# Optimization experiments

Hardware: AMD Instinct MI355X
Metric: run time of the kernel (lower is better)

Reference implementation:

```python
import jax, jax.numpy as jnp
import numpy as np


def setup_inputs() -> dict:
    key = jax.random.key(0)
    ks = jax.random.split(key, 7)
    B, D, d1, d2, d3 = 256, 256, 1024, 512, 256
    s = lambda f: 1.0 / np.sqrt(f)  # torch nn.Linear-style init scale
    return {
        "x": jax.random.normal(ks[0], (B, D), jnp.float32),
        "W1": jax.random.normal(ks[1], (d1, D), jnp.float32) * s(D),
        "b1": jax.random.normal(ks[2], (d1,), jnp.float32) * s(D),
        "W2": jax.random.normal(ks[3], (d2, d1), jnp.float32) * s(d1),
        "b2": jax.random.normal(ks[4], (d2,), jnp.float32) * s(d1),
        "W3": jax.random.normal(ks[5], (d3, d2), jnp.float32) * s(d2),
        "b3": jax.random.normal(ks[6], (d3,), jnp.float32) * s(d2),
        "k": 10,
    }


def _border_dists(x, W1, b1, W2, b2, W3, b3):
    # Layer 1: pre-activations and boundary distances. For the first layer the
    # effective linear map is W1 itself (shared across the batch).
    z1 = x @ W1.T + b1                                   # [B, d1]
    dist1 = jnp.abs(z1) / jnp.linalg.norm(W1, axis=1)    # [B, d1]
    m1 = (z1 > 0).astype(x.dtype)
    V1 = m1[:, :, None] * W1[None]                       # [B, d1, D] per-instance map after ReLU
    h1 = m1 * z1

    # Layer 2
    z2 = h1 @ W2.T + b2                                  # [B, d2]
    V2 = jnp.einsum('oi,bid->bod', W2, V1)               # [B, d2, D]
    dist2 = jnp.abs(z2) / jnp.linalg.norm(V2, axis=2)
    m2 = (z2 > 0).astype(x.dtype)
    h2 = m2 * z2

    # Layer 3
    z3 = h2 @ W3.T + b3                                  # [B, d3]
    V3 = jnp.einsum('oi,bid->bod', W3, m2[:, :, None] * V2)  # [B, d3, D]
    dist3 = jnp.abs(z3) / jnp.linalg.norm(V3, axis=2)

    return jnp.concatenate([dist1, dist2, dist3], axis=1)  # [B, d1+d2+d3]


def reference(x, W1, b1, W2, b2, W3, b3, k):
    dists = _border_dists(x, W1, b1, W2, b2, W3, b3)
    # smallest-k distances per instance via top_k on negated distances
    neg_top, _ = jax.lax.top_k(-dists, k)                # [B, k]
    return jnp.sum(-neg_top)                             # border-distance loss (scalar)
```

## Files before the change

kernel.cpp:

```cpp
#include <hip/hip_runtime.h>
#include <math.h>
#include <float.h>

#define B   256
#define D   256
#define D1  1024
#define D2  512
#define D3  256
#define NDIST (D1 + D2 + D3)
#define CQ  2.0f

typedef __attribute__((ext_vector_type(8))) short short8;
typedef __attribute__((ext_vector_type(4))) float f32x4;
typedef __attribute__((ext_vector_type(4))) int   i32x4;

__device__ __forceinline__ float waveReduceSum(float v) {
    #pragma unroll
    for (int off = 32; off > 0; off >>= 1)
        v += __shfl_down(v, off, 64);
    return v;
}
__device__ __forceinline__ float waveReduceMax(float v) {
    #pragma unroll
    for (int off = 32; off > 0; off >>= 1)
        v = fmaxf(v, __shfl_down(v, off, 64));
    return v;
}
__device__ __forceinline__ unsigned short f2bf(float f) {
    unsigned int u = __float_as_uint(f);
    u = (u + 0x7FFFu + ((u >> 16) & 1u)) >> 16;
    return (unsigned short)u;
}
__device__ __forceinline__ float bf2f(unsigned short h) {
    return __uint_as_float(((unsigned int)h) << 16);
}
__device__ __forceinline__ void gld16(const void* g, void* l) {
    __builtin_amdgcn_global_load_lds(
        (const __attribute__((address_space(1))) unsigned int*)g,
        (__attribute__((address_space(3))) unsigned int*)l, 16, 0, 0);
}
__device__ __forceinline__ int swz_src(int row, int lane) {
    return ((lane & 3) + ((row >> 1) & 3)) & 3;
}
__device__ __forceinline__ int swz_frag(int row, int quad) {
    return row * 32 + (((quad - ((row >> 1) & 3)) & 3) * 8);
}

__device__ __forceinline__ void split8(const float* p, short8& h8, short8& l8) {
    float4 a = *(const float4*)(p);
    float4 b = *(const float4*)(p + 4);
    float hv[8] = { a.x, a.y, a.z, a.w, b.x, b.y, b.z, b.w };
    #pragma unroll
    for (int q = 0; q < 8; q++) {
        unsigned short hh = f2bf(hv[q]);
        h8[q] = (short)hh;
        l8[q] = (short)f2bf(hv[q] - bf2f(hh));
    }
}

template <int KD, int KL>
__device__ __forceinline__ void mfma3_64(
    const unsigned short* __restrict__ Ahi, const unsigned short* __restrict__ Alo,
    const unsigned short* __restrict__ Bhi, const unsigned short* __restrict__ Blo,
    int m0, int n0, int k0, unsigned short* sm, f32x4 acc[2][2]) {
    int tid = threadIdx.x;
    int l = tid & 63, w = tid >> 6;
    int rsub = l >> 2;
    int quad = l >> 4, l16 = l & 15;
    int wm = (w >> 1) * 32, wn = (w & 1) * 32;
    unsigned short* sAh = sm;
    unsigned short* sAl = sm + 2048;
    unsigned short* sBh = sm + 4096;
    unsigned short* sBl = sm + 6144;
    ptrdiff_t dA = Alo - Ahi, dB = Blo - Bhi;
    int rloc = w * 16 + rsub;
    int c = swz_src(rloc, l);
    const unsigned short* pa = Ahi + (size_t)(m0 + rloc) * KD + k0 + c * 8;
    const unsigned short* pb = Bhi + (size_t)(n0 + rloc) * KD + k0 + c * 8;
    int aoff[2], boff[2];
    #pragma unroll
    for (int mt = 0; mt < 2; mt++) aoff[mt] = swz_frag(wm + mt * 16 + l16, quad);
    #pragma unroll
    for (int nt = 0; nt < 2; nt++) boff[nt] = swz_frag(wn + nt * 16 + l16, quad);
    for (int kk = 0; kk < KL; kk += 32) {
        gld16(pa + kk,      sAh + w * 512);
        gld16(pa + dA + kk, sAl + w * 512);
        gld16(pb + kk,      sBh + w * 512);
        gld16(pb + dB + kk, sBl + w * 512);
        __syncthreads();
        short8 ah[2], al[2], bh[2], bl[2];
        #pragma unroll
        for (int mt = 0; mt < 2; mt++) {
            ah[mt] = *(const short8*)(sAh + aoff[mt]);
            al[mt] = *(const short8*)(sAl + aoff[mt]);
        }
        #pragma unroll
        for (int nt = 0; nt < 2; nt++) {
            bh[nt] = *(const short8*)(sBh + boff[nt]);
            bl[nt] = *(const short8*)(sBl + boff[nt]);
        }
        #pragma unroll
        for (int mt = 0; mt < 2; mt++)
            #pragma unroll
            for (int nt = 0; nt < 2; nt++) {
                acc[mt][nt] = __builtin_amdgcn_mfma_f32_16x16x32_bf16(ah[mt], bh[nt], acc[mt][nt], 0, 0, 0);
                acc[mt][nt] = __builtin_amdgcn_mfma_f32_16x16x32_bf16(ah[mt], bl[nt], acc[mt][nt], 0, 0, 0);
                acc[mt][nt] = __builtin_amdgcn_mfma_f32_16x16x32_bf16(al[mt], bh[nt], acc[mt][nt], 0, 0, 0);
            }
        __syncthreads();
    }
}

__global__ __launch_bounds__(256) void k_l1p(
    const float* __restrict__ x, const float* __restrict__ W1,
    const float* __restrict__ W2, const float* __restrict__ W3,
    const float* __restrict__ b1,
    float* __restrict__ dists, unsigned char* __restrict__ m1q,
    unsigned short* __restrict__ h1hi, unsigned short* __restrict__ h1lo,
    float* __restrict__ zeros, float* __restrict__ outp,
    unsigned short* __restrict__ W2hi, unsigned short* __restrict__ W2lo,
    unsigned short* __restrict__ W3hi, unsigned short* __restrict__ W3lo,
    signed char* __restrict__ W1Ti8, float* __restrict__ saq,
    signed char* __restrict__ W2i8,  float* __restrict__ sbq,
    signed char* __restrict__ W3i8,  float* __restrict__ s3q,
    float* __restrict__ rn1) {
    __shared__ __align__(16) unsigned short sm[8192];
    int blk = blockIdx.x;
    int t = threadIdx.x;

    if (blk < 64) {
        unsigned short* sAh = sm;
        unsigned short* sAl = sm + 2048;
        unsigned short* sBh = sm + 4096;
        unsigned short* sBl = sm + 6144;
        int m0 = (blk & 3) * 64, n0 = (blk >> 2) * 64;
        int l = t & 63, w = t >> 6;
        int rsub = l >> 2;
        int quad = l >> 4, l16 = l & 15;
        int wm = (w >> 1) * 32, wn = (w & 1) * 32;
        int rloc = w * 16 + rsub;
        int c = swz_src(rloc, l);
        const float* pax = x + (size_t)(m0 + rloc) * D + c * 8;
        const float* pbw = W1 + (size_t)(n0 + rloc) * D + c * 8;
        int aoff[2], boff[2];
        #pragma unroll
        for (int mt = 0; mt < 2; mt++) aoff[mt] = swz_frag(wm + mt * 16 + l16, quad);
        #pragma unroll
        for (int nt = 0; nt < 2; nt++) boff[nt] = swz_frag(wn + nt * 16 + l16, quad);
        int wrA = w * 512 + l * 8;
        f32x4 acc[2][2] = {};
        for (int kk = 0; kk < D; kk += 32) {
            short8 ha, la, hb, lb;
            split8(pax + kk, ha, la);
            split8(pbw + kk, hb, lb);
            *(short8*)(sAh + wrA) = ha;
            *(short8*)(sAl + wrA) = la;
            *(short8*)(sBh + wrA) = hb;
            *(short8*)(sBl + wrA) = lb;
            __syncthreads();
            short8 ah[2], al[2], bh[2], bl[2];
            #pragma unroll
            for (int mt = 0; mt < 2; mt++) {
                ah[mt] = *(const short8*)(sAh + aoff[mt]);
                al[mt] = *(const short8*)(sAl + aoff[mt]);
            }
            #pragma unroll
            for (int nt = 0; nt < 2; nt++) {
                bh[nt] = *(const short8*)(sBh + boff[nt]);
                bl[nt] = *(const short8*)(sBl + boff[nt]);
            }
            #pragma unroll
            for (int mt = 0; mt < 2; mt++)
                #pragma unroll
                for (int nt = 0; nt < 2; nt++) {
                    acc[mt][nt] = __builtin_amdgcn_mfma_f32_16x16x32_bf16(ah[mt], bh[nt], acc[mt][nt], 0, 0, 0);
                    acc[mt][nt] = __builtin_amdgcn_mfma_f32_16x16x32_bf16(ah[mt], bl[nt], acc[mt][nt], 0, 0, 0);
                    acc[mt][nt] = __builtin_amdgcn_mfma_f32_16x16x32_bf16(al[mt], bh[nt], acc[mt][nt], 0, 0, 0);
                }
            __syncthreads();
        }
        #pragma unroll
        for (int mt = 0; mt < 2; mt++)
            #pragma unroll
            for (int nt = 0; nt < 2; nt++) {
                int n = n0 + wn + nt * 16 + l16;
                float bv = b1[n];
                #pragma unroll
                for (int r = 0; r < 4; r++) {
                    int m = m0 + wm + mt * 16 + quad * 4 + r;
                    float z = acc[mt][nt][r] + bv;
                    size_t idx = (size_t)m * D1 + n;
                    dists[idx] = fabsf(z);
                    m1q[idx] = (z > 0.f) ? 0xFFu : 0u;
                    float h = z > 0.f ? z : 0.f;
                    unsigned short hh = f2bf(h);
                    h1hi[idx] = hh;
                    h1lo[idx] = f2bf(h - bf2f(hh));
                }
            }
        return;
    }
    if (blk < 448) {
        if (blk == 64 && t == 0) outp[0] = 0.f;
        int i4 = (blk - 64) * 1024 + t * 4;
        *(float4*)(zeros + i4) = make_float4(0.f, 0.f, 0.f, 0.f);
        return;
    }
    if (blk < 480) {
        int ty = t >> 5, tx = t & 31;
        int d = (blk - 448) * 8 + ty;
        float m = 0.f;
        for (int i = tx; i < D1; i += 32) m = fmaxf(m, fabsf(W1[(size_t)i * D + d]));
        #pragma unroll
        for (int off = 16; off > 0; off >>= 1) m = fmaxf(m, __shfl_down(m, off, 32));
        m = __shfl(m, 0, 32);
        m = fmaxf(m, 1e-20f);
        if (tx == 0) saq[d] = m / 127.f;
        float inv = 127.f / m;
        for (int i = tx; i < D1; i += 32) {
            int q = __float2int_rn(W1[(size_t)i * D + d] * inv);
            W1Ti8[(size_t)d * D1 + i] = (signed char)q;
        }
        return;
    }
    if (blk < 608) {
        int o = (blk - 480) * 4 + (t >> 6);
        int l = t & 63;
        const float* row = W2 + (size_t)o * D1;
        float4 v[4];
        #pragma unroll
        for (int jj = 0; jj < 4; jj++) v[jj] = *(const float4*)(row + jj * 256 + l * 4);
        float m = 0.f;
        #pragma unroll
        for (int jj = 0; jj < 4; jj++)
            m = fmaxf(m, fmaxf(fmaxf(fabsf(v[jj].x), fabsf(v[jj].y)),
                               fmaxf(fabsf(v[jj].z), fabsf(v[jj].w))));
        m = waveReduceMax(m);
        m = __shfl(m, 0, 64);
        m = fmaxf(m, 1e-20f);
        if (l == 0) sbq[o] = m / 127.f;
        float inv = 127.f / m;
        #pragma unroll
        for (int jj = 0; jj < 4; jj++) {
            int base = jj * 256 + l * 4;
            int q0 = __float2int_rn(v[jj].x * inv);
            int q1 = __float2int_rn(v[jj].y * inv);
            int q2 = __float2int_rn(v[jj].z * inv);
            int q3 = __float2int_rn(v[jj].w * inv);
            unsigned int pk = (unsigned)(q0 & 255) | ((unsigned)(q1 & 255) << 8) |
                              ((unsigned)(q2 & 255) << 16) | ((unsigned)(q3 & 255) << 24);
            *(unsigned int*)(W2i8 + (size_t)o * D1 + base) = pk;
            ushort4 h, lo;
            h.x = f2bf(v[jj].x); lo.x = f2bf(v[jj].x - bf2f(h.x));
            h.y = f2bf(v[jj].y); lo.y = f2bf(v[jj].y - bf2f(h.y));
            h.z = f2bf(v[jj].z); lo.z = f2bf(v[jj].z - bf2f(h.z));
            h.w = f2bf(v[jj].w); lo.w = f2bf(v[jj].w - bf2f(h.w));
            *(ushort4*)(W2hi + (size_t)o * D1 + base) = h;
            *(ushort4*)(W2lo + (size_t)o * D1 + base) = lo;
        }
        return;
    }
    if (blk < 672) {
        int p = (blk - 608) * 4 + (t >> 6);
        int l = t & 63;
        const float* row = W3 + (size_t)p * D2;
        float4 v[2];
        #pragma unroll
        for (int jj = 0; jj < 2; jj++) v[jj] = *(const float4*)(row + jj * 256 + l * 4);
        float m = 0.f;
        #pragma unroll
        for (int jj = 0; jj < 2; jj++)
            m = fmaxf(m, fmaxf(fmaxf(fabsf(v[jj].x), fabsf(v[jj].y)),
                               fmaxf(fabsf(v[jj].z), fabsf(v[jj].w))));
        m = waveReduceMax(m);
        m = __shfl(m, 0, 64);
        m = fmaxf(m, 1e-20f);
        if (l == 0) s3q[p] = m / 127.f;
        float inv = 127.f / m;
        #pragma unroll
        for (int jj = 0; jj < 2; jj++) {
            int base = jj * 256 + l * 4;
            int q0 = __float2int_rn(v[jj].x * inv);
            int q1 = __float2int_rn(v[jj].y * inv);
            int q2 = __float2int_rn(v[jj].z * inv);
            int q3 = __float2int_rn(v[jj].w * inv);
            unsigned int pk = (unsigned)(q0 & 255) | ((unsigned)(q1 & 255) << 8) |
                              ((unsigned)(q2 & 255) << 16) | ((unsigned)(q3 & 255) << 24);
            *(unsigned int*)(W3i8 + (size_t)p * D2 + base) = pk;
            ushort4 h, lo;
            h.x = f2bf(v[jj].x); lo.x = f2bf(v[jj].x - bf2f(h.x));
            h.y = f2bf(v[jj].y); lo.y = f2bf(v[jj].y - bf2f(h.y));
            h.z = f2bf(v[jj].z); lo.z = f2bf(v[jj].z - bf2f(h.z));
            h.w = f2bf(v[jj].w); lo.w = f2bf(v[jj].w - bf2f(h.w));
            *(ushort4*)(W3hi + (size_t)p * D2 + base) = h;
            *(ushort4*)(W3lo + (size_t)p * D2 + base) = lo;
        }
        return;
    }
    {
        int gw = (blk - 672) * 4 + (t >> 6);
        int lane = t & 63;
        const float* row = W1 + (size_t)gw * D;
        float s = 0.f;
        for (int tt = lane; tt < D; tt += 64) { float v = row[tt]; s += v * v; }
        s = waveReduceSum(s);
        if (lane == 0) rn1[gw] = sqrtf(s);
    }
}

__global__ __launch_bounds__(256, 2) void k_big1(
    const unsigned short* __restrict__ h1hi, const unsigned short* __restrict__ h1lo,
    const unsigned short* __restrict__ W2hi, const unsigned short* __restrict__ W2lo,
    float* __restrict__ z2,
    const signed char* __restrict__ W1Ti8,
    const signed char* __restrict__ W2i8,
    const unsigned char* __restrict__ m1q,
    const float* __restrict__ saq,
    const float* __restrict__ sbq,
    signed char* __restrict__ qV2,
    float* __restrict__ norm2) {
    __shared__ __align__(16) unsigned char smem[34816];
    int bid = blockIdx.x;

    if (bid < 128) {
        unsigned short* sm = (unsigned short*)smem;
        int m0 = (bid & 3) * 64, n0 = ((bid >> 2) & 7) * 64, k0 = (bid >> 5) * 256;
        f32x4 acc[2][2] = {};
        mfma3_64<D1, 256>(h1hi, h1lo, W2hi, W2lo, m0, n0, k0, sm, acc);
        int l = threadIdx.x & 63, w = threadIdx.x >> 6;
        int quad = l >> 4, l16 = l & 15;
        int wm = (w >> 1) * 32, wn = (w & 1) * 32;
        #pragma unroll
        for (int mt = 0; mt < 2; mt++)
            #pragma unroll
            for (int nt = 0; nt < 2; nt++) {
                int n = n0 + wn + nt * 16 + l16;
                #pragma unroll
                for (int r = 0; r < 4; r++) {
                    int m = m0 + wm + mt * 16 + quad * 4 + r;
                    atomicAdd(&z2[(size_t)m * D2 + n], acc[mt][nt][r]);
                }
            }
        return;
    }

    int j = bid - 128;
    signed char* As = (signed char*)smem;
    signed char* Bs = (signed char*)smem + 16384;
    unsigned char* mbuf = (unsigned char*)smem + 32768;
    int m0 = (j & 1) * 128;
    int o0 = ((j >> 1) & 3) * 128;
    int b0 = (j >> 3) * 2;
    int tid = threadIdx.x;
    int l = tid & 63, w = tid >> 6;
    int quad = l >> 4, l16 = l & 15;
    int wm = (w >> 1) * 64, wn = (w & 1) * 64;

    *(int2*)(mbuf + tid * 8) = *(const int2*)(m1q + (size_t)b0 * D1 + tid * 8);

    const signed char* pa[4];
    const signed char* pb[4];
    int lrow = l >> 3, ls = l & 7;
    #pragma unroll
    for (int r = 0; r < 4; r++) {
        int row = r * 32 + w * 8 + lrow;
        int c = (ls + (row & 7)) & 7;
        pa[r] = W1Ti8 + (size_t)(m0 + row) * D1 + c * 16;
        pb[r] = W2i8 + (size_t)(o0 + row) * D1 + c * 16;
    }
    int aoff[4][2], boff[4][2];
    #pragma unroll
    for (int mt = 0; mt < 4; mt++) {
        int tr = wm + mt * 16 + l16;
        #pragma unroll
        for (int ks = 0; ks < 2; ks++)
            aoff[mt][ks] = tr * 128 + (((ks * 4 + quad) - (tr & 7)) & 7) * 16;
    }
    #pragma unroll
    for (int nt = 0; nt < 4; nt++) {
        int tr = wn + nt * 16 + l16;
        #pragma unroll
        for (int ks = 0; ks < 2; ks++)
            boff[nt][ks] = tr * 128 + (((ks * 4 + quad) - (tr & 7)) & 7) * 16;
    }

    i32x4 acc[2][4][4];
    #pragma unroll
    for (int g = 0; g < 2; g++)
        #pragma unroll
        for (int i = 0; i < 4; i++)
            #pragma unroll
            for (int jj = 0; jj < 4; jj++) acc[g][i][jj] = (i32x4)0;

    for (int t = 0; t < 8; t++) {
        int kk = t * 128;
        #pragma unroll
        for (int r = 0; r < 4; r++) {
            gld16(pa[r] + kk, As + r * 4096 + w * 1024);
            gld16(pb[r] + kk, Bs + r * 4096 + w * 1024);
        }
        __syncthreads();
        #pragma unroll
        for (int ks = 0; ks < 2; ks++) {
            i32x4 mva = *(const i32x4*)(mbuf +        t * 128 + ks * 64 + quad * 16);
            i32x4 mvb = *(const i32x4*)(mbuf + 1024 + t * 128 + ks * 64 + quad * 16);
            i32x4 a[4], bq[4];
            #pragma unroll
            for (int mt = 0; mt < 4; mt++)
                a[mt] = *(const i32x4*)(As + aoff[mt][ks]);
            #pragma unroll
            for (int nt = 0; nt < 4; nt++)
                bq[nt] = *(const i32x4*)(Bs + boff[nt][ks]);
            #pragma unroll
            for (int mt = 0; mt < 4; mt++) {
                i32x4 a0 = a[mt] & mva;
                i32x4 a1 = a[mt] & mvb;
                #pragma unroll
                for (int nt = 0; nt < 4; nt++)
                    acc[0][mt][nt] = __builtin_amdgcn_mfma_i32_16x16x64_i8(
                        a0, bq[nt], acc[0][mt][nt], 0, 0, 0);
                #pragma unroll
                for (int nt = 0; nt < 4; nt++)
                    acc[1][mt][nt] = __builtin_amdgcn_mfma_i32_16x16x64_i8(
                        a1, bq[nt], acc[1][mt][nt], 0, 0, 0);
            }
        }
        __syncthreads();
    }

    float sad[4][4];
    #pragma unroll
    for (int mt = 0; mt < 4; mt++)
        #pragma unroll
        for (int r = 0; r < 4; r++)
            sad[mt][r] = saq[m0 + wm + mt * 16 + quad * 4 + r];
    float sbv[4], sbdq[4];
    #pragma unroll
    for (int nt = 0; nt < 4; nt++) {
        sbv[nt] = sbq[o0 + wn + nt * 16 + l16];
        sbdq[nt] = sbv[nt] * (1.0f / CQ);
    }

    #pragma unroll
    for (int g = 0; g < 2; g++) {
        int bg = b0 + g;
        float nrm[4] = {0.f, 0.f, 0.f, 0.f};
        signed char* qb = qV2 + (size_t)bg * (D * D2);
        #pragma unroll
        for (int mt = 0; mt < 4; mt++) {
            int dbase = m0 + wm + mt * 16 + quad * 4;
            #pragma unroll
            for (int r = 0; r < 4; r++) {
                float sa = sad[mt][r];
                size_t rowoff = (size_t)(dbase + r) * D2;
                #pragma unroll
                for (int nt = 0; nt < 4; nt++) {
                    float tv = (float)acc[g][mt][nt][r];
                    float u = tv * sa;
                    nrm[nt] = fmaf(u, u, nrm[nt]);
                    int qi = __float2int_rn(tv * sbdq[nt]);
                    qi = max(-127, min(127, qi));
                    qb[rowoff + o0 + wn + nt * 16 + l16] = (signed char)qi;
                }
            }
        }
        #pragma unroll
        for (int nt = 0; nt < 4; nt++) {
            float s = nrm[nt] * (sbv[nt] * sbv[nt]);
            s += __shfl_down(s, 32, 64);
            s += __shfl_down(s, 16, 64);
            if (l < 16)
                atomicAdd(&norm2[(size_t)bg * D2 + o0 + wn + nt * 16 + l], s);
        }
    }
}

__global__ __launch_bounds__(256) void k_big2(
    const float* __restrict__ z2,
    const float* __restrict__ b2,
    const unsigned short* __restrict__ W3hi, const unsigned short* __restrict__ W3lo,
    float* __restrict__ z3,
    const signed char* __restrict__ W3i8,
    const signed char* __restrict__ qV2,
    const float* __restrict__ saq,
    const float* __restrict__ s3q,
    float* __restrict__ norm3) {
    __shared__ __align__(16) unsigned char smem[33280];
    int bid = blockIdx.x;
    int tid = threadIdx.x;

    if (bid < 32) {
        unsigned short* sAh = (unsigned short*)smem;
        unsigned short* sAl = sAh + 2048;
        unsigned short* sBh = sAh + 4096;
        unsigned short* sBl = sAh + 6144;
        int m0 = (bid & 3) * 64, n0 = ((bid >> 2) & 3) * 64, k0 = (bid >> 4) * 256;
        int l = tid & 63, w = tid >> 6;
        int rsub = l >> 2;
        int quad = l >> 4, l16 = l & 15;
        int wm = (w >> 1) * 32, wn = (w & 1) * 32;
        int rloc = w * 16 + rsub;
        int c = swz_src(rloc, l);
        const float* pz  = z2 + (size_t)(m0 + rloc) * D2 + k0 + c * 8;
        const float* pbi = b2 + k0 + c * 8;
        const unsigned short* pb = W3hi + (size_t)(n0 + rloc) * D2 + k0 + c * 8;
        ptrdiff_t dB = W3lo - W3hi;
        int aoff[2], boff[2];
        #pragma unroll
        for (int mt = 0; mt < 2; mt++) aoff[mt] = swz_frag(wm + mt * 16 + l16, quad);
        #pragma unroll
        for (int nt = 0; nt < 2; nt++) boff[nt] = swz_frag(wn + nt * 16 + l16, quad);
        int wrA = w * 512 + l * 8;
        f32x4 acc[2][2] = {};
        for (int kk = 0; kk < 256; kk += 32) {
            gld16(pb + kk,      sBh + w * 512);
            gld16(pb + dB + kk, sBl + w * 512);
            float4 za = *(const float4*)(pz + kk);
            float4 zb = *(const float4*)(pz + kk + 4);
            float4 ba = *(const float4*)(pbi + kk);
            float4 bb = *(const float4*)(pbi + kk + 4);
            float hv[8] = { za.x + ba.x, za.y + ba.y, za.z + ba.z, za.w + ba.w,
                            zb.x + bb.x, zb.y + bb.y, zb.z + bb.z, zb.w + bb.w };
            short8 h8, l8;
            #pragma unroll
            for (int q2 = 0; q2 < 8; q2++) {
                float h = hv[q2] > 0.f ? hv[q2] : 0.f;
                unsigned short hh = f2bf(h);
                h8[q2] = (short)hh;
                l8[q2] = (short)f2bf(h - bf2f(hh));
            }
            *(short8*)(sAh + wrA) = h8;
            *(short8*)(sAl + wrA) = l8;
            __syncthreads();
            short8 ah[2], al[2], bh[2], bl[2];
            #pragma unroll
            for (int mt = 0; mt < 2; mt++) {
                ah[mt] = *(const short8*)(sAh + aoff[mt]);
                al[mt] = *(const short8*)(sAl + aoff[mt]);
            }
            #pragma unroll
            for (int nt = 0; nt < 2; nt++) {
                bh[nt] = *(const short8*)(sBh + boff[nt]);
                bl[nt] = *(const short8*)(sBl + boff[nt]);
            }
            #pragma unroll
            for (int mt = 0; mt < 2; mt++)
                #pragma unroll
                for (int nt = 0; nt < 2; nt++) {
                    acc[mt][nt] = __builtin_amdgcn_mfma_f32_16x16x32_bf16(ah[mt], bh[nt], acc[mt][nt], 0, 0, 0);
                    acc[mt][nt] = __builtin_amdgcn_mfma_f32_16x16x32_bf16(ah[mt], bl[nt], acc[mt][nt], 0, 0, 0);
                    acc[mt][nt] = __builtin_amdgcn_mfma_f32_16x16x32_bf16(al[mt], bh[nt], acc[mt][nt], 0, 0, 0);
                }
            __syncthreads();
        }
        #pragma unroll
        for (int mt = 0; mt < 2; mt++)
            #pragma unroll
            for (int nt = 0; nt < 2; nt++) {
                int n = n0 + wn + nt * 16 + l16;
                #pragma unroll
                for (int r = 0; r < 4; r++) {
                    int m = m0 + wm + mt * 16 + quad * 4 + r;
                    atomicAdd(&z3[(size_t)m * D3 + n], acc[mt][nt][r]);
                }
            }
        return;
    }

    int j = bid - 32;
    signed char* As = (signed char*)smem;
    signed char* Bs = (signed char*)smem + 16384;
    unsigned char* mbuf = (unsigned char*)smem + 32768;
    int m0 = (j & 1) * 128;
    int n0 = ((j >> 1) & 1) * 128;
    int bc = j >> 2;
    int l = tid & 63, w = tid >> 6;
    int quad = l >> 4, l16 = l & 15;
    int wm = (w >> 1) * 64, wn = (w & 1) * 64;
    const signed char* Bsrc = qV2 + (size_t)bc * (D * D2);

    {
        #pragma unroll
        for (int rr = 0; rr < 2; rr++) {
            int o = tid * 2 + rr;
            float z = z2[(size_t)bc * D2 + o] + b2[o];
            mbuf[o] = (z > 0.f) ? 0xFFu : 0u;
        }
    }
    __syncthreads();

    const signed char* pa[4];
    const signed char* pb[4];
    int lrow = l >> 3, ls = l & 7;
    #pragma unroll
    for (int r = 0; r < 4; r++) {
        int row = r * 32 + w * 8 + lrow;
        int c = (ls + (row & 7)) & 7;
        pa[r] = W3i8 + (size_t)(m0 + row) * D2 + c * 16;
        pb[r] = Bsrc + (size_t)(n0 + row) * D2 + c * 16;
    }
    int aoff[4][2], boff[4][2];
    #pragma unroll
    for (int mt = 0; mt < 4; mt++) {
        int tr = wm + mt * 16 + l16;
        #pragma unroll
        for (int ks = 0; ks < 2; ks++)
            aoff[mt][ks] = tr * 128 + (((ks * 4 + quad) - (tr & 7)) & 7) * 16;
    }
    #pragma unroll
    for (int nt = 0; nt < 4; nt++) {
        int tr = wn + nt * 16 + l16;
        #pragma unroll
        for (int ks = 0; ks < 2; ks++)
            boff[nt][ks] = tr * 128 + (((ks * 4 + quad) - (tr & 7)) & 7) * 16;
    }

    i32x4 acc[4][4];
    #pragma unroll
    for (int i = 0; i < 4; i++)
        #pragma unroll
        for (int jj = 0; jj < 4; jj++) acc[i][jj] = (i32x4)0;

    for (int kk = 0; kk < D2; kk += 128) {
        #pragma unroll
        for (int r = 0; r < 4; r++) {
            gld16(pa[r] + kk, As + r * 4096 + w * 1024);
            gld16(pb[r] + kk, Bs + r * 4096 + w * 1024);
        }
        __syncthreads();
        i32x4 mv0 = *(const i32x4*)(mbuf + kk + quad * 16);
        i32x4 mv1 = *(const i32x4*)(mbuf + kk + 64 + quad * 16);
        #pragma unroll
        for (int ks = 0; ks < 2; ks++) {
            i32x4 mv = ks ? mv1 : mv0;
            i32x4 a[4], bq[4];
            #pragma unroll
            for (int mt = 0; mt < 4; mt++)
                a[mt] = *(const i32x4*)(As + aoff[mt][ks]);
            #pragma unroll
            for (int nt = 0; nt < 4; nt++)
                bq[nt] = (*(const i32x4*)(Bs + boff[nt][ks])) & mv;
            #pragma unroll
            for (int mt = 0; mt < 4; mt++)
                #pragma unroll
                for (int nt = 0; nt < 4; nt++)
                    acc[mt][nt] = __builtin_amdgcn_mfma_i32_16x16x64_i8(
                        a[mt], bq[nt], acc[mt][nt], 0, 0, 0);
        }
        __syncthreads();
    }

    float saCQ[4];
    #pragma unroll
    for (int nt = 0; nt < 4; nt++)
        saCQ[nt] = saq[n0 + wn + nt * 16 + l16] * CQ;

    #pragma unroll
    for (int mt = 0; mt < 4; mt++)
        #pragma unroll
        for (int r = 0; r < 4; r++) {
            float s = 0.f;
            #pragma unroll
            for (int nt = 0; nt < 4; nt++) {
                float v = (float)acc[mt][nt][r] * saCQ[nt];
                s += v * v;
            }
            s += __shfl_down(s, 8, 64);
            s += __shfl_down(s, 4, 64);
            s += __shfl_down(s, 2, 64);
            s += __shfl_down(s, 1, 64);
            if (l16 == 0) {
                int p = m0 + wm + mt * 16 + quad * 4 + r;
                float s3 = s3q[p];
                atomicAdd(&norm3[(size_t)bc * D3 + p], s * s3 * s3);
            }
        }
}

__global__ __launch_bounds__(256) void k_topk(
    const float* __restrict__ dists,
    const float* __restrict__ rn1,
    const float* __restrict__ z2, const float* __restrict__ b2,
    const float* __restrict__ norm2,
    const float* __restrict__ z3, const float* __restrict__ b3,
    const float* __restrict__ norm3,
    const int* __restrict__ kp, float* __restrict__ outp) {
    int t = threadIdx.x;
    int wv = t >> 6, lane = t & 63;
    int b = blockIdx.x * 4 + wv;
    float lv[28];
    #pragma unroll
    for (int j = 0; j < 16; j++) {
        int n = lane + 64 * j;
        lv[j] = dists[(size_t)b * D1 + n] / rn1[n];
    }
    #pragma unroll
    for (int j = 16; j < 24; j++) {
        int o = lane + 64 * (j - 16);
        float zz = z2[(size_t)b * D2 + o] + b2[o];
        lv[j] = fabsf(zz) / sqrtf(norm2[(size_t)b * D2 + o]);
    }
    #pragma unroll
    for (int j = 24; j < 28; j++) {
        int p = lane + 64 * (j - 24);
        float zz = z3[(size_t)b * D3 + p] + b3[p];
        lv[j] = fabsf(zz) / sqrtf(norm3[(size_t)b * D3 + p]);
    }
    int k = *kp;
    if (k > NDIST) k = NDIST;
    float sum = 0.f;
    for (int it = 0; it < k; it++) {
        float mv = lv[0]; int mj = 0;
        #pragma unroll
        for (int j = 1; j < 28; j++)
            if (lv[j] < mv) { mv = lv[j]; mj = j; }
        unsigned long long key =
            ((unsigned long long)__float_as_uint(mv) << 32) | (unsigned)(lane * 32 + mj);
        #pragma unroll
        for (int off = 1; off < 64; off <<= 1) {
            unsigned long long o = __shfl_xor(key, off, 64);
            if (o < key) key = o;
        }
        sum += __uint_as_float((unsigned)(key >> 32));
        int wl = (int)((key >> 5) & 63u), wj = (int)(key & 31u);
        if (lane == wl) lv[wj] = FLT_MAX;
    }
    if (lane == 0) atomicAdd(outp, sum);
}

extern "C" void kernel_launch(void* const* d_in, const int* in_sizes, int n_in,
                              void* d_out, int out_size, void* d_ws, size_t ws_size,
                              hipStream_t stream) {
    const float* x  = (const float*)d_in[0];
    const float* W1 = (const float*)d_in[1];
    const float* b1 = (const float*)d_in[2];
    const float* W2 = (const float*)d_in[3];
    const float* b2 = (const float*)d_in[4];
    const float* W3 = (const float*)d_in[5];
    const float* b3 = (const float*)d_in[6];
    const int*   kp = (const int*)d_in[7];
    float* outp = (float*)d_out;

    float* fp = (float*)d_ws;
    float* rn1     = fp;                          fp += D1;
    float* dists   = fp;                          fp += (size_t)B * D1;
    float* saq     = fp;                          fp += D;
    float* sbq     = fp;                          fp += D2;
    float* s3q     = fp;                          fp += D3;
    float* z2      = fp;                          fp += (size_t)B * D2;
    float* z3      = fp;                          fp += (size_t)B * D3;
    float* norm2   = fp;                          fp += (size_t)B * D2;
    float* norm3   = fp;                          fp += (size_t)B * D3;
    unsigned short* up = (unsigned short*)fp;
    unsigned short* W2hi  = up;  up += (size_t)D2 * D1;
    unsigned short* W2lo  = up;  up += (size_t)D2 * D1;
    unsigned short* W3hi  = up;  up += (size_t)D3 * D2;
    unsigned short* W3lo  = up;  up += (size_t)D3 * D2;
    unsigned short* h1hi  = up;  up += (size_t)B * D1;
    unsigned short* h1lo  = up;  up += (size_t)B * D1;
    signed char*    cp = (signed char*)up;
    signed char*    W1Ti8 = cp;  cp += (size_t)D * D1;
    signed char*    W2i8  = cp;  cp += (size_t)D2 * D1;
    signed char*    W3i8  = cp;  cp += (size_t)D3 * D2;
    unsigned char*  m1q   = (unsigned char*)cp;  cp += (size_t)B * D1;
    signed char*    qV2   = cp;

    k_l1p<<<928, 256, 0, stream>>>(x, W1, W2, W3, b1,
                                   dists, m1q, h1hi, h1lo,
                                   z2, outp, W2hi, W2lo, W3hi, W3lo,
                                   W1Ti8, saq, W2i8, sbq, W3i8, s3q, rn1);

    k_big1<<<1152, 256, 0, stream>>>(h1hi, h1lo, W2hi, W2lo, z2,
                                     W1Ti8, W2i8, m1q, saq, sbq, qV2, norm2);

    k_big2<<<1056, 256, 0, stream>>>(z2, b2, W3hi, W3lo, z3,
                                     W3i8, qV2, saq, s3q, norm3);

    k_topk<<<B / 4, 256, 0, stream>>>(dists, rn1, z2, b2, norm2, z3, b3, norm3,
                                      kp, outp);
}
```

Before: 161.8 us.

## Enlarge k_big1 V2 tile to 128x256 with 512-thread blocks

```diff
diff --git a/kernel.cpp b/kernel.cpp
--- a/kernel.cpp
+++ b/kernel.cpp
@@ -308,7 +308,7 @@
     }
 }
 
-__global__ __launch_bounds__(256, 2) void k_big1(
+__global__ __launch_bounds__(512, 1) void k_big1(
     const unsigned short* __restrict__ h1hi, const unsigned short* __restrict__ h1lo,
     const unsigned short* __restrict__ W2hi, const unsigned short* __restrict__ W2lo,
     float* __restrict__ z2,
@@ -319,53 +319,106 @@
     const float* __restrict__ sbq,
     signed char* __restrict__ qV2,
     float* __restrict__ norm2) {
-    __shared__ __align__(16) unsigned char smem[34816];
+    __shared__ __align__(16) unsigned char smem[51200];
     int bid = blockIdx.x;
+    int tid = threadIdx.x;
+    int l = tid & 63, w = tid >> 6;
+    int quad = l >> 4, l16 = l & 15;
 
     if (bid < 128) {
-        unsigned short* sm = (unsigned short*)smem;
+        bool act = (w < 4);
+        int w4 = w & 3;
+        unsigned short* sAh = (unsigned short*)smem;
+        unsigned short* sAl = sAh + 2048;
+        unsigned short* sBh = sAh + 4096;
+        unsigned short* sBl = sAh + 6144;
         int m0 = (bid & 3) * 64, n0 = ((bid >> 2) & 7) * 64, k0 = (bid >> 5) * 256;
+        int rsub = l >> 2;
+        int wm = (w4 >> 1) * 32, wn = (w4 & 1) * 32;
+        ptrdiff_t dA = h1lo - h1hi, dB = W2lo - W2hi;
+        int rloc = w4 * 16 + rsub;
+        int c = swz_src(rloc, l);
+        const unsigned short* pa = h1hi + (size_t)(m0 + rloc) * D1 + k0 + c * 8;
+        const unsigned short* pb = W2hi + (size_t)(n0 + rloc) * D2 * 2 + k0 + c * 8;
+        pb = W2hi + (size_t)(n0 + rloc) * D1 + k0 + c * 8;
+        int aoff[2], boff[2];
+        #pragma unroll
+        for (int mt = 0; mt < 2; mt++) aoff[mt] = swz_frag(wm + mt * 16 + l16, quad);
+        #pragma unroll
+        for (int nt = 0; nt < 2; nt++) boff[nt] = swz_frag(wn + nt * 16 + l16, quad);
         f32x4 acc[2][2] = {};
-        mfma3_64<D1, 256>(h1hi, h1lo, W2hi, W2lo, m0, n0, k0, sm, acc);
-        int l = threadIdx.x & 63, w = threadIdx.x >> 6;
-        int quad = l >> 4, l16 = l & 15;
-        int wm = (w >> 1) * 32, wn = (w & 1) * 32;
-        #pragma unroll
-        for (int mt = 0; mt < 2; mt++)
-            #pragma unroll
-            for (int nt = 0; nt < 2; nt++) {
-                int n = n0 + wn + nt * 16 + l16;
-                #pragma unroll
-                for (int r = 0; r < 4; r++) {
-                    int m = m0 + wm + mt * 16 + quad * 4 + r;
-                    atomicAdd(&z2[(size_t)m * D2 + n], acc[mt][nt][r]);
+        for (int kk = 0; kk < 256; kk += 32) {
+            if (act) {
+                gld16(pa + kk,      sAh + w4 * 512);
+                gld16(pa + dA + kk, sAl + w4 * 512);
+                gld16(pb + kk,      sBh + w4 * 512);
+                gld16(pb + dB + kk, sBl + w4 * 512);
+            }
+            __syncthreads();
+            if (act) {
+                short8 ah[2], al[2], bh[2], bl[2];
+                #pragma unroll
+                for (int mt = 0; mt < 2; mt++) {
+                    ah[mt] = *(const short8*)(sAh + aoff[mt]);
+                    al[mt] = *(const short8*)(sAl + aoff[mt]);
                 }
-            }
+                #pragma unroll
+                for (int nt = 0; nt < 2; nt++) {
+                    bh[nt] = *(const short8*)(sBh + boff[nt]);
+                    bl[nt] = *(const short8*)(sBl + boff[nt]);
+                }
+                #pragma unroll
+                for (int mt = 0; mt < 2; mt++)
+                    #pragma unroll
+                    for (int nt = 0; nt < 2; nt++) {
+                        acc[mt][nt] = __builtin_amdgcn_mfma_f32_16x16x32_bf16(ah[mt], bh[nt], acc[mt][nt], 0, 0, 0);
+                        acc[mt][nt] = __builtin_amdgcn_mfma_f32_16x16x32_bf16(ah[mt], bl[nt], acc[mt][nt], 0, 0, 0);
+                        acc[mt][nt] = __builtin_amdgcn_mfma_f32_16x16x32_bf16(al[mt], bh[nt], acc[mt][nt], 0, 0, 0);
+                    }
+            }
+            __syncthreads();
+        }
+        if (act) {
+            #pragma unroll
+            for (int mt = 0; mt < 2; mt++)
+                #pragma unroll
+                for (int nt = 0; nt < 2; nt++) {
+                    int n = n0 + wn + nt * 16 + l16;
+                    #pragma unroll
+                    for (int r = 0; r < 4; r++) {
+                        int m = m0 + wm + mt * 16 + quad * 4 + r;
+                        atomicAdd(&z2[(size_t)m * D2 + n], acc[mt][nt][r]);
+                    }
+                }
+        }
         return;
     }
 
     int j = bid - 128;
     signed char* As = (signed char*)smem;
     signed char* Bs = (signed char*)smem + 16384;
-    unsigned char* mbuf = (unsigned char*)smem + 32768;
+    unsigned char* mbuf = (unsigned char*)smem + 49152;
     int m0 = (j & 1) * 128;
-    int o0 = ((j >> 1) & 3) * 128;
-    int b0 = (j >> 3) * 2;
-    int tid = threadIdx.x;
-    int l = tid & 63, w = tid >> 6;
-    int quad = l >> 4, l16 = l & 15;
-    int wm = (w >> 1) * 64, wn = (w & 1) * 64;
-
-    *(int2*)(mbuf + tid * 8) = *(const int2*)(m1q + (size_t)b0 * D1 + tid * 8);
-
-    const signed char* pa[4];
+    int o0 = ((j >> 1) & 1) * 256;
+    int b0 = (j >> 2) * 2;
+    int wm = (w >> 2) * 64;
+    int wn = (w & 3) * 64;
+
+    *(int*)(mbuf + tid * 4) = *(const int*)(m1q + (size_t)b0 * D1 + tid * 4);
+
+    const signed char* pa[2];
     const signed char* pb[4];
     int lrow = l >> 3, ls = l & 7;
     #pragma unroll
-    for (int r = 0; r < 4; r++) {
-        int row = r * 32 + w * 8 + lrow;
+    for (int r = 0; r < 2; r++) {
+        int row = r * 64 + w * 8 + lrow;
         int c = (ls + (row & 7)) & 7;
         pa[r] = W1Ti8 + (size_t)(m0 + row) * D1 + c * 16;
+    }
+    #pragma unroll
+    for (int r = 0; r < 4; r++) {
+        int row = r * 64 + w * 8 + lrow;
+        int c = (ls + (row & 7)) & 7;
         pb[r] = W2i8 + (size_t)(o0 + row) * D1 + c * 16;
     }
     int aoff[4][2], boff[4][2];
@@ -395,10 +448,11 @@
     for (int t = 0; t < 8; t++) {
         int kk = t * 128;
         #pragma unroll
-        for (int r = 0; r < 4; r++) {
-            gld16(pa[r] + kk, As + r * 4096 + w * 1024);
-            gld16(pb[r] + kk, Bs + r * 4096 + w * 1024);
-        }
+        for (int r = 0; r < 2; r++)
+            gld16(pa[r] + kk, As + r * 8192 + w * 1024);
+        #pragma unroll
+        for (int r = 0; r < 4; r++)
+            gld16(pb[r] + kk, Bs + r * 8192 + w * 1024);
         __syncthreads();
         #pragma unroll
         for (int ks = 0; ks < 2; ks++) {
@@ -770,8 +824,8 @@
                                    z2, outp, W2hi, W2lo, W3hi, W3lo,
                                    W1Ti8, saq, W2i8, sbq, W3i8, s3q, rn1);
 
-    k_big1<<<1152, 256, 0, stream>>>(h1hi, h1lo, W2hi, W2lo, z2,
-                                     W1Ti8, W2i8, m1q, saq, sbq, qV2, norm2);
+    k_big1<<<640, 512, 0, stream>>>(h1hi, h1lo, W2hi, W2lo, z2,
+                                    W1Ti8, W2i8, m1q, saq, sbq, qV2, norm2);
 
     k_big2<<<1056, 256, 0, stream>>>(z2, b2, W3hi, W3lo, z3,
                                      W3i8, qV2, saq, s3q, norm3);
```

Result: slower. 168.1 us (+3.9%).

## Process two batch instances per block in k_big2 to reuse W3 tiles

Applied to the files above, without the earlier changes.

```diff
diff --git a/kernel.cpp b/kernel.cpp
--- a/kernel.cpp
+++ b/kernel.cpp
@@ -475,7 +475,7 @@
     }
 }
 
-__global__ __launch_bounds__(256) void k_big2(
+__global__ __launch_bounds__(256, 2) void k_big2(
     const float* __restrict__ z2,
     const float* __restrict__ b2,
     const unsigned short* __restrict__ W3hi, const unsigned short* __restrict__ W3lo,
@@ -485,7 +485,7 @@
     const float* __restrict__ saq,
     const float* __restrict__ s3q,
     float* __restrict__ norm3) {
-    __shared__ __align__(16) unsigned char smem[33280];
+    __shared__ __align__(16) unsigned char smem[50176];
     int bid = blockIdx.x;
     int tid = threadIdx.x;
 
@@ -568,36 +568,41 @@
     }
 
     int j = bid - 32;
-    signed char* As = (signed char*)smem;
-    signed char* Bs = (signed char*)smem + 16384;
-    unsigned char* mbuf = (unsigned char*)smem + 32768;
+    signed char* As  = (signed char*)smem;
+    signed char* Bs0 = (signed char*)smem + 16384;
+    signed char* Bs1 = (signed char*)smem + 32768;
+    unsigned char* mbuf = (unsigned char*)smem + 49152;
     int m0 = (j & 1) * 128;
     int n0 = ((j >> 1) & 1) * 128;
-    int bc = j >> 2;
+    int bc0 = (j >> 2) * 2;
     int l = tid & 63, w = tid >> 6;
     int quad = l >> 4, l16 = l & 15;
     int wm = (w >> 1) * 64, wn = (w & 1) * 64;
-    const signed char* Bsrc = qV2 + (size_t)bc * (D * D2);
+    const signed char* Bsrc0 = qV2 + (size_t)bc0 * (D * D2);
+    const signed char* Bsrc1 = Bsrc0 + (size_t)(D * D2);
 
     {
         #pragma unroll
         for (int rr = 0; rr < 2; rr++) {
             int o = tid * 2 + rr;
-            float z = z2[(size_t)bc * D2 + o] + b2[o];
-            mbuf[o] = (z > 0.f) ? 0xFFu : 0u;
-        }
-    }
-    __syncthreads();
+            float za = z2[(size_t)bc0 * D2 + o] + b2[o];
+            float zb = z2[(size_t)(bc0 + 1) * D2 + o] + b2[o];
+            mbuf[o]       = (za > 0.f) ? 0xFFu : 0u;
+            mbuf[512 + o] = (zb > 0.f) ? 0xFFu : 0u;
+        }
+    }
 
     const signed char* pa[4];
-    const signed char* pb[4];
+    const signed char* pb0[4];
+    const signed char* pb1[4];
     int lrow = l >> 3, ls = l & 7;
     #pragma unroll
     for (int r = 0; r < 4; r++) {
         int row = r * 32 + w * 8 + lrow;
         int c = (ls + (row & 7)) & 7;
-        pa[r] = W3i8 + (size_t)(m0 + row) * D2 + c * 16;
-        pb[r] = Bsrc + (size_t)(n0 + row) * D2 + c * 16;
+        pa[r]  = W3i8  + (size_t)(m0 + row) * D2 + c * 16;
+        pb0[r] = Bsrc0 + (size_t)(n0 + row) * D2 + c * 16;
+        pb1[r] = Bsrc1 + (size_t)(n0 + row) * D2 + c * 16;
     }
     int aoff[4][2], boff[4][2];
     #pragma unroll
@@ -615,37 +620,51 @@
             boff[nt][ks] = tr * 128 + (((ks * 4 + quad) - (tr & 7)) & 7) * 16;
     }
 
-    i32x4 acc[4][4];
-    #pragma unroll
-    for (int i = 0; i < 4; i++)
-        #pragma unroll
-        for (int jj = 0; jj < 4; jj++) acc[i][jj] = (i32x4)0;
-
-    for (int kk = 0; kk < D2; kk += 128) {
+    i32x4 acc[2][4][4];
+    #pragma unroll
+    for (int g = 0; g < 2; g++)
+        #pragma unroll
+        for (int i = 0; i < 4; i++)
+            #pragma unroll
+            for (int jj = 0; jj < 4; jj++) acc[g][i][jj] = (i32x4)0;
+
+    for (int t = 0; t < 4; t++) {
+        int kk = t * 128;
         #pragma unroll
         for (int r = 0; r < 4; r++) {
-            gld16(pa[r] + kk, As + r * 4096 + w * 1024);
-            gld16(pb[r] + kk, Bs + r * 4096 + w * 1024);
+            gld16(pa[r]  + kk, As  + r * 4096 + w * 1024);
+            gld16(pb0[r] + kk, Bs0 + r * 4096 + w * 1024);
+            gld16(pb1[r] + kk, Bs1 + r * 4096 + w * 1024);
         }
         __syncthreads();
-        i32x4 mv0 = *(const i32x4*)(mbuf + kk + quad * 16);
-        i32x4 mv1 = *(const i32x4*)(mbuf + kk + 64 + quad * 16);
+        i32x4 mv0a = *(const i32x4*)(mbuf + kk + quad * 16);
+        i32x4 mv1a = *(const i32x4*)(mbuf + kk + 64 + quad * 16);
+        i32x4 mv0b = *(const i32x4*)(mbuf + 512 + kk + quad * 16);
+        i32x4 mv1b = *(const i32x4*)(mbuf + 512 + kk + 64 + quad * 16);
         #pragma unroll
         for (int ks = 0; ks < 2; ks++) {
-            i32x4 mv = ks ? mv1 : mv0;
-            i32x4 a[4], bq[4];
+            i32x4 mva = ks ? mv1a : mv0a;
+            i32x4 mvb = ks ? mv1b : mv0b;
+            i32x4 a[4], bqa[4], bqb[4];
             #pragma unroll
             for (int mt = 0; mt < 4; mt++)
                 a[mt] = *(const i32x4*)(As + aoff[mt][ks]);
             #pragma unroll
-            for (int nt = 0; nt < 4; nt++)
-                bq[nt] = (*(const i32x4*)(Bs + boff[nt][ks])) & mv;
-            #pragma unroll
-            for (int mt = 0; mt < 4; mt++)
+            for (int nt = 0; nt < 4; nt++) {
+                bqa[nt] = (*(const i32x4*)(Bs0 + boff[nt][ks])) & mva;
+                bqb[nt] = (*(const i32x4*)(Bs1 + boff[nt][ks])) & mvb;
+            }
+            #pragma unroll
+            for (int mt = 0; mt < 4; mt++) {
                 #pragma unroll
                 for (int nt = 0; nt < 4; nt++)
-                    acc[mt][nt] = __builtin_amdgcn_mfma_i32_16x16x64_i8(
-                        a[mt], bq[nt], acc[mt][nt], 0, 0, 0);
+                    acc[0][mt][nt] = __builtin_amdgcn_mfma_i32_16x16x64_i8(
+                        a[mt], bqa[nt], acc[0][mt][nt], 0, 0, 0);
+                #pragma unroll
+                for (int nt = 0; nt < 4; nt++)
+                    acc[1][mt][nt] = __builtin_amdgcn_mfma_i32_16x16x64_i8(
+                        a[mt], bqb[nt], acc[1][mt][nt], 0, 0, 0);
+            }
         }
         __syncthreads();
     }
@@ -656,25 +675,29 @@
         saCQ[nt] = saq[n0 + wn + nt * 16 + l16] * CQ;
 
     #pragma unroll
-    for (int mt = 0; mt < 4; mt++)
-        #pragma unroll
-        for (int r = 0; r < 4; r++) {
-            float s = 0.f;
-            #pragma unroll
-            for (int nt = 0; nt < 4; nt++) {
-                float v = (float)acc[mt][nt][r] * saCQ[nt];
-                s += v * v;
-            }
-            s += __shfl_down(s, 8, 64);
-            s += __shfl_down(s, 4, 64);
-            s += __shfl_down(s, 2, 64);
-            s += __shfl_down(s, 1, 64);
-            if (l16 == 0) {
-                int p = m0 + wm + mt * 16 + quad * 4 + r;
-                float s3 = s3q[p];
-                atomicAdd(&norm3[(size_t)bc * D3 + p], s * s3 * s3);
-            }
-        }
+    for (int g = 0; g < 2; g++) {
+        int bg = bc0 + g;
+        #pragma unroll
+        for (int mt = 0; mt < 4; mt++)
+            #pragma unroll
+            for (int r = 0; r < 4; r++) {
+                float s = 0.f;
+                #pragma unroll
+                for (int nt = 0; nt < 4; nt++) {
+                    float v = (float)acc[g][mt][nt][r] * saCQ[nt];
+                    s += v * v;
+                }
+                s += __shfl_down(s, 8, 64);
+                s += __shfl_down(s, 4, 64);
+                s += __shfl_down(s, 2, 64);
+                s += __shfl_down(s, 1, 64);
+                if (l16 == 0) {
+                    int p = m0 + wm + mt * 16 + quad * 4 + r;
+                    float s3 = s3q[p];
+                    atomicAdd(&norm3[(size_t)bg * D3 + p], s * s3 * s3);
+                }
+            }
+    }
 }
 
 __global__ __launch_bounds__(256) void k_topk(
@@ -773,8 +796,8 @@
     k_big1<<<1152, 256, 0, stream>>>(h1hi, h1lo, W2hi, W2lo, z2,
                                      W1Ti8, W2i8, m1q, saq, sbq, qV2, norm2);
 
-    k_big2<<<1056, 256, 0, stream>>>(z2, b2, W3hi, W3lo, z3,
-                                     W3i8, qV2, saq, s3q, norm3);
+    k_big2<<<544, 256, 0, stream>>>(z2, b2, W3hi, W3lo, z3,
+                                    W3i8, qV2, saq, s3q, norm3);
 
     k_topk<<<B / 4, 256, 0, stream>>>(dists, rn1, z2, b2, norm2, z3, b3, norm3,
                                       kp, outp);
```

Measured after the change: 166.1 us. +2.6%, slower.
